# Performance work log

Hardware: AMD Instinct MI355X
Metric: run time of the kernel (lower is better)

Reference implementation:

```python
import jax, jax.numpy as jnp
import numpy as np

B, C, H, W, HEADS = 4, 32, 384, 384, 8
EPS_LN = 1e-6


def conv2d(x, w, b=None, pad=0, groups=1):
    out = jax.lax.conv_general_dilated(
        x, w, window_strides=(1, 1), padding=[(pad, pad), (pad, pad)],
        dimension_numbers=('NCHW', 'OIHW', 'NCHW'), feature_group_count=groups)
    return out if b is None else out + b[None, :, None, None]


def setup_inputs() -> dict:
    key = jax.random.key(0)
    ks = jax.random.split(key, 24)
    p = lambda k, shape: jax.random.normal(k, shape, jnp.float32) * 0.05
    return {
        'x': jax.random.normal(ks[0], (B, C, H, W), jnp.float32),
        # MCC core params (bias=False)
        'ln_w': jnp.ones((C,), jnp.float32),
        'ln_b': jnp.zeros((C,), jnp.float32),
        'temperature': jnp.ones((HEADS, 1, 1), jnp.float32),
        'pw_w': p(ks[1], (3 * C, C, 1, 1)),
        'dw_w': p(ks[2], (3 * C, 1, 3, 3)),
        'proj_w': p(ks[3], (C, C, 1, 1)),
        'ff1_w': p(ks[4], (C, C, 1, 1)),
        'ffdw_w': p(ks[5], (C, 1, 3, 3)),
        # color-space detector (convs have default bias=True)
        'det_w1': p(ks[6], (64, 32, 3, 3)), 'det_b1': jnp.zeros((64,), jnp.float32),
        'det_w2': p(ks[7], (128, 64, 3, 3)), 'det_b2': jnp.zeros((128,), jnp.float32),
        'det_w3': p(ks[8], (256, 128, 3, 3)), 'det_b3': jnp.zeros((256,), jnp.float32),
        'det_fc_w': p(ks[9], (3, 256)), 'det_fc_b': jnp.zeros((3,), jnp.float32),
        # HVI->RGB model
        'hvi_w1': p(ks[10], (64, 32, 3, 3)), 'hvi_b1': jnp.zeros((64,), jnp.float32),
        'hvi_w2': p(ks[11], (32, 64, 3, 3)), 'hvi_b2': jnp.zeros((32,), jnp.float32),
        # YCbCr->RGB model
        'ycc_w1': p(ks[12], (64, 32, 3, 3)), 'ycc_b1': jnp.zeros((64,), jnp.float32),
        'ycc_w2': p(ks[13], (32, 64, 3, 3)), 'ycc_b2': jnp.zeros((32,), jnp.float32),
    }


def _mcc_forward(x, ln_w, ln_b, temperature, pw_w, dw_w, proj_w, ff1_w, ffdw_w,
                 det_w1, det_b1, det_w2, det_b2, det_w3, det_b3, det_fc_w, det_fc_b,
                 hvi_w1, hvi_b1, hvi_w2, hvi_b2, ycc_w1, ycc_b1, ycc_w2, ycc_b2):
    relu = jax.nn.relu
    # ---- auto color-space detection ----
    f = relu(conv2d(x, det_w1, det_b1, pad=1))
    f = relu(conv2d(f, det_w2, det_b2, pad=1))
    f = relu(conv2d(f, det_w3, det_b3, pad=1))
    f = f.mean(axis=(2, 3))                      # adaptive avg pool -> [B, 256]
    logits = f @ det_fc_w.T + det_fc_b           # [B, 3]
    pred = jnp.argmax(logits[0])                 # torch uses predicted[0].item()

    def rgb_branch(xx):
        return xx

    def hvi_branch(xx):
        return relu(conv2d(relu(conv2d(xx, hvi_w1, hvi_b1, pad=1)), hvi_w2, hvi_b2, pad=1))

    def ycc_branch(xx):
        return relu(conv2d(relu(conv2d(xx, ycc_w1, ycc_b1, pad=1)), ycc_w2, ycc_b2, pad=1))

    x = jax.lax.switch(pred, [rgb_branch, hvi_branch, ycc_branch], x)

    # ---- channels_first LayerNorm ----
    u = x.mean(axis=1, keepdims=True)
    s = ((x - u) ** 2).mean(axis=1, keepdims=True)
    a = (x - u) / jnp.sqrt(s + EPS_LN)
    a = ln_w[None, :, None, None] * a + ln_b[None, :, None, None]

    # ---- qkv: 1x1 pwconv then 3x3 depthwise ----
    qkv = conv2d(conv2d(a, pw_w, pad=0), dw_w, pad=1, groups=3 * C)  # [B, 3C, H, W]
    q, k, v = jnp.split(qkv, 3, axis=1)
    ch = C // HEADS                                # channels per head
    hw = H * W
    q = q.reshape(B, HEADS, ch, hw)
    k = k.reshape(B, HEADS, ch, hw)
    v = v.reshape(B, HEADS, ch, hw)
    # L2-normalize over spatial dim (F.normalize, eps=1e-12)
    q = q / jnp.maximum(jnp.linalg.norm(q, axis=-1, keepdims=True), 1e-12)
    k = k / jnp.maximum(jnp.linalg.norm(k, axis=-1, keepdims=True), 1e-12)
    # channel-wise transposed attention: [B, heads, ch, ch]
    attn = jnp.einsum('bhcn,bhdn->bhcd', q, k) * temperature
    attn = jax.nn.softmax(attn, axis=-1)
    out = jnp.einsum('bhcd,bhdn->bhcn', attn, v).reshape(B, C, H, W)
    out = conv2d(out, proj_w, pad=0)

    # ---- feedforward on residual ----
    y = out + x
    y = jax.nn.gelu(conv2d(y, ff1_w, pad=0), approximate=False)
    y = jax.nn.gelu(conv2d(y, ffdw_w, pad=1, groups=C), approximate=False)
    return y


def reference(x, ln_w, ln_b, temperature, pw_w, dw_w, proj_w, ff1_w, ffdw_w,
              det_w1, det_b1, det_w2, det_b2, det_w3, det_b3, det_fc_w, det_fc_b,
              hvi_w1, hvi_b1, hvi_w2, hvi_b2, ycc_w1, ycc_b1, ycc_w2, ycc_b2):
    return _mcc_forward(x, ln_w, ln_b, temperature, pw_w, dw_w, proj_w, ff1_w, ffdw_w,
                        det_w1, det_b1, det_w2, det_b2, det_w3, det_b3, det_fc_w, det_fc_b,
                        hvi_w1, hvi_b1, hvi_w2, hvi_b2, ycc_w1, ycc_b1, ycc_w2, ycc_b2)
```

## Files before the change

### kernel.cpp

```cpp
#include <hip/hip_runtime.h>
#include <hip/hip_bf16.h>
#include <math.h>

#define HH 384
#define WW 384
#define HWSZ (HH*WW)
#define BB 4

typedef __attribute__((ext_vector_type(8))) short short8;
typedef __attribute__((ext_vector_type(4))) float f32x4;

static const size_t OFF_MISC = 0;
static const size_t OFF_A    = 16384;
static const size_t OFF_BW   = OFF_A + 56623104;
static const size_t MISC_POOLED = 0;
static const size_t MISC_PRED   = 1024;
static const size_t MISC_STATS  = 1056;
static const size_t MISC_MB     = 2048;

#define LPAD 40

__device__ __forceinline__ float waveSum(float v) {
#pragma unroll
    for (int off = 32; off > 0; off >>= 1) v += __shfl_down(v, off);
    return v;
}

__device__ __forceinline__ float gelu_exact(float v) {
    return 0.5f * v * (1.0f + erff(v * 0.70710678118654752f));
}

__device__ __forceinline__ unsigned short f2bf(float f) {
    __hip_bfloat16 h = __float2bfloat16(f);
    return *(unsigned short*)&h;
}
__device__ __forceinline__ float bf2f(unsigned short u) {
    unsigned int b = ((unsigned int)u) << 16;
    return __uint_as_float(b);
}

__device__ __forceinline__ void dwconv8(const float* __restrict__ base,
                                        const float* __restrict__ w9,
                                        int y, int xg, float o[8])
{
#pragma unroll
    for (int j = 0; j < 8; ++j) o[j] = 0.f;
#pragma unroll
    for (int dy = 0; dy < 3; ++dy) {
        int gy = y + dy - 1;
        if ((unsigned)gy >= (unsigned)HH) continue;
        const float* rp = base + (size_t)gy * WW + xg;
        f32x4 m0 = *(const f32x4*)(rp);
        f32x4 m1 = *(const f32x4*)(rp + 4);
        float r0 = (xg > 0) ? rp[-1] : 0.f;
        float r9 = (xg + 8 < WW) ? rp[8] : 0.f;
        float r[10] = {r0, m0[0], m0[1], m0[2], m0[3],
                           m1[0], m1[1], m1[2], m1[3], r9};
        float w0 = w9[dy * 3 + 0], w1 = w9[dy * 3 + 1], w2 = w9[dy * 3 + 2];
#pragma unroll
        for (int j = 0; j < 8; ++j)
            o[j] = fmaf(r[j], w0, fmaf(r[j + 1], w1, fmaf(r[j + 2], w2, o[j])));
    }
}


__global__ __launch_bounds__(256) void xcvt_kernel(
    const float* __restrict__ x, unsigned short* __restrict__ x0)
{
    int px = blockIdx.x * 256 + threadIdx.x;
    if (px >= HWSZ) return;
    unsigned short u[32];
#pragma unroll
    for (int c = 0; c < 32; ++c) u[c] = f2bf(x[(size_t)c * HWSZ + px]);
    uint4* dst = (uint4*)(x0 + (size_t)px * 32);
#pragma unroll
    for (int g = 0; g < 4; ++g) {
        uint4 v;
        v.x = (unsigned)u[g*8+0] | ((unsigned)u[g*8+1] << 16);
        v.y = (unsigned)u[g*8+2] | ((unsigned)u[g*8+3] << 16);
        v.z = (unsigned)u[g*8+4] | ((unsigned)u[g*8+5] << 16);
        v.w = (unsigned)u[g*8+6] | ((unsigned)u[g*8+7] << 16);
        dst[g] = v;
    }
}

__global__ __launch_bounds__(256) void wcvt_kernel(
    const float* __restrict__ w, unsigned short* __restrict__ wp,
    int Cin, int total)
{
    int t = blockIdx.x * 256 + threadIdx.x;
    if (t >= total) return;
    int nine_cin = 9 * Cin;
    int co = t / nine_cin;
    int r = t - co * nine_cin;
    int e = r / Cin;
    int ci = r - e * Cin;
    wp[t] = f2bf(w[(size_t)co * nine_cin + ci * 9 + e]);
}

template<int CIN, int COUT>
__global__ __launch_bounds__(256) void mfma_conv2_kernel(
    const unsigned short* __restrict__ in,
    const unsigned short* __restrict__ wp,
    const float* __restrict__ bias,
    unsigned short* __restrict__ out)
{
    constexpr int NT = COUT / 64;
    __shared__ unsigned short s_in[198 * LPAD];

    const int tid  = threadIdx.x;
    const int lane = tid & 63;
    const int wave = tid >> 6;
    const int nl   = lane & 15;
    const int quad = lane >> 4;
    const int row  = blockIdx.x / 6;
    const int x0   = (blockIdx.x % 6) * 64;
    const int co_w0 = wave * (COUT / 4);

    f32x4 acc[4][NT];
#pragma unroll
    for (int pg = 0; pg < 4; ++pg)
#pragma unroll
        for (int ct = 0; ct < NT; ++ct) acc[pg][ct] = (f32x4){0.f,0.f,0.f,0.f};

#pragma unroll
    for (int ci0 = 0; ci0 < CIN; ci0 += 32) {
        __syncthreads();
        for (int idx = tid; idx < 792; idx += 256) {
            int qs   = idx & 3;
            int cell = idx >> 2;
            int px   = cell % 66;
            int r    = cell / 66;
            int gy   = row + r - 1;
            int gx   = x0 + px - 1;
            uint4 v = {0u,0u,0u,0u};
            if ((unsigned)gy < (unsigned)HH && (unsigned)gx < (unsigned)WW)
                v = *(const uint4*)(in + (size_t)(gy * WW + gx) * CIN + ci0 + qs * 8);
            *(uint4*)(s_in + cell * LPAD + qs * 8) = v;
        }
        __syncthreads();
#pragma unroll
        for (int e = 0; e < 9; ++e) {
            const int er = e / 3, ec = e % 3;
            short8 bfrag[4];
#pragma unroll
            for (int pg = 0; pg < 4; ++pg)
                bfrag[pg] = *(const short8*)(s_in + ((er * 66 + pg * 16 + nl + ec) * LPAD + quad * 8));
#pragma unroll
            for (int ct = 0; ct < NT; ++ct) {
                short8 afrag = *(const short8*)(wp
                    + (size_t)(co_w0 + ct * 16 + nl) * (9 * CIN) + e * CIN + ci0 + quad * 8);
#pragma unroll
                for (int pg = 0; pg < 4; ++pg)
                    acc[pg][ct] = __builtin_amdgcn_mfma_f32_16x16x32_bf16(afrag, bfrag[pg], acc[pg][ct], 0, 0, 0);
            }
        }
    }

#pragma unroll
    for (int pg = 0; pg < 4; ++pg) {
        int px = x0 + pg * 16 + nl;
        unsigned short* op = out + ((size_t)row * WW + px) * COUT;
#pragma unroll
        for (int ct = 0; ct < NT; ++ct) {
            int cb = co_w0 + ct * 16 + quad * 4;
            ushort4 v;
            v.x = f2bf(fmaxf(acc[pg][ct][0] + bias[cb + 0], 0.f));
            v.y = f2bf(fmaxf(acc[pg][ct][1] + bias[cb + 1], 0.f));
            v.z = f2bf(fmaxf(acc[pg][ct][2] + bias[cb + 2], 0.f));
            v.w = f2bf(fmaxf(acc[pg][ct][3] + bias[cb + 3], 0.f));
            *(ushort4*)(op + cb) = v;
        }
    }
}

__global__ __launch_bounds__(256) void pool_kernel(
    const unsigned short* __restrict__ d3, float* __restrict__ pooled)
{
    __shared__ float s_pool[256];
    int t = threadIdx.x;
    s_pool[t] = 0.f;
    __syncthreads();
    int co8 = (t & 31) * 8;
    int pxg = t >> 5;
    float sums[8];
#pragma unroll
    for (int j = 0; j < 8; ++j) sums[j] = 0.f;
    int base = blockIdx.x * 2304 + pxg;
    for (int i = 0; i < 288; ++i) {
        int px = base + i * 8;
        const uint4* p = (const uint4*)(d3 + (size_t)px * 256 + co8);
        uint4 v = *p;
        unsigned int w[4] = {v.x, v.y, v.z, v.w};
#pragma unroll
        for (int g = 0; g < 4; ++g) {
            sums[g*2+0] += bf2f((unsigned short)(w[g] & 0xFFFF));
            sums[g*2+1] += bf2f((unsigned short)(w[g] >> 16));
        }
    }
#pragma unroll
    for (int j = 0; j < 8; ++j) atomicAdd(&s_pool[co8 + j], sums[j]);
    __syncthreads();
    atomicAdd(&pooled[t], s_pool[t]);
}

__global__ void fc_argmax_kernel(const float* __restrict__ pooled,
                                 const float* __restrict__ fcw,
                                 const float* __restrict__ fcb,
                                 int* __restrict__ pred)
{
    int t = threadIdx.x;
    float m = pooled[t] * (1.0f / (float)HWSZ);
    float p0 = m * fcw[t];
    float p1 = m * fcw[256 + t];
    float p2 = m * fcw[512 + t];
    p0 = waveSum(p0); p1 = waveSum(p1); p2 = waveSum(p2);
    __shared__ float rr[3][4];
    int wid = t >> 6, lane = t & 63;
    if (lane == 0) { rr[0][wid] = p0; rr[1][wid] = p1; rr[2][wid] = p2; }
    __syncthreads();
    if (t == 0) {
        float l0 = rr[0][0] + rr[0][1] + rr[0][2] + rr[0][3] + fcb[0];
        float l1 = rr[1][0] + rr[1][1] + rr[1][2] + rr[1][3] + fcb[1];
        float l2 = rr[2][0] + rr[2][1] + rr[2][2] + rr[2][3] + fcb[2];
        int best = 0; float bv = l0;
        if (l1 > bv) { best = 1; bv = l1; }
        if (l2 > bv) { best = 2; bv = l2; }
        *pred = best;
    }
}


__global__ __launch_bounds__(256) void wsplit_kernel(
    const float* __restrict__ w,
    unsigned short* __restrict__ hi, unsigned short* __restrict__ lo,
    int Cin, int total)
{
    int t = blockIdx.x * 256 + threadIdx.x;
    if (t >= total) return;
    int nine_cin = 9 * Cin;
    int co = t / nine_cin;
    int r = t - co * nine_cin;
    int e = r / Cin;
    int ci = r - e * Cin;
    float v = w[(size_t)co * nine_cin + ci * 9 + e];
    unsigned short h = f2bf(v);
    hi[t] = h;
    lo[t] = f2bf(v - bf2f(h));
}

__global__ __launch_bounds__(256) void xsplitb_kernel(
    const float* __restrict__ x, const int* __restrict__ predp,
    unsigned short* __restrict__ hi, unsigned short* __restrict__ lo)
{
    if (__builtin_amdgcn_readfirstlane(*predp) == 0) return;
    int p = blockIdx.x * 256 + threadIdx.x;
    if (p >= BB * HWSZ) return;
    int b = p / HWSZ, n = p % HWSZ;
    const float* sp = x + (size_t)b * 32 * HWSZ + n;
    unsigned short uh[32], ul[32];
#pragma unroll
    for (int c = 0; c < 32; ++c) {
        float v = sp[(size_t)c * HWSZ];
        unsigned short h = f2bf(v);
        uh[c] = h;
        ul[c] = f2bf(v - bf2f(h));
    }
    uint4* dh = (uint4*)(hi + (size_t)p * 32);
    uint4* dl = (uint4*)(lo + (size_t)p * 32);
#pragma unroll
    for (int g = 0; g < 4; ++g) {
        uint4 vh, vl;
        vh.x = (unsigned)uh[g*8+0] | ((unsigned)uh[g*8+1] << 16);
        vh.y = (unsigned)uh[g*8+2] | ((unsigned)uh[g*8+3] << 16);
        vh.z = (unsigned)uh[g*8+4] | ((unsigned)uh[g*8+5] << 16);
        vh.w = (unsigned)uh[g*8+6] | ((unsigned)uh[g*8+7] << 16);
        vl.x = (unsigned)ul[g*8+0] | ((unsigned)ul[g*8+1] << 16);
        vl.y = (unsigned)ul[g*8+2] | ((unsigned)ul[g*8+3] << 16);
        vl.z = (unsigned)ul[g*8+4] | ((unsigned)ul[g*8+5] << 16);
        vl.w = (unsigned)ul[g*8+6] | ((unsigned)ul[g*8+7] << 16);
        dh[g] = vh;
        dl[g] = vl;
    }
}

template<int CIN, int COUT, int OUTMODE>
__global__ __launch_bounds__(256) void bconv_kernel(
    const unsigned short* __restrict__ in_hi, const unsigned short* __restrict__ in_lo,
    const unsigned short* __restrict__ wAh, const unsigned short* __restrict__ wAl,
    const unsigned short* __restrict__ wBh, const unsigned short* __restrict__ wBl,
    const float* __restrict__ bA, const float* __restrict__ bB,
    const int* __restrict__ predp,
    unsigned short* __restrict__ out_hi, unsigned short* __restrict__ out_lo,
    float* __restrict__ out_f32)
{
    const int p = __builtin_amdgcn_readfirstlane(*predp);
    if (p == 0) return;
    const unsigned short* whi = (p == 1) ? wAh : wBh;
    const unsigned short* wlo = (p == 1) ? wAl : wBl;
    const float* bias = (p == 1) ? bA : bB;

    constexpr int NPG = (COUT == 64) ? 4 : 2;
    __shared__ unsigned short s_hi[198 * LPAD];
    __shared__ unsigned short s_lo[198 * LPAD];

    const int tid  = threadIdx.x;
    const int lane = tid & 63;
    const int wave = tid >> 6;
    const int nl   = lane & 15;
    const int quad = lane >> 4;
    const int row  = blockIdx.x / 6;
    const int x0   = (blockIdx.x % 6) * 64;
    const int b    = blockIdx.y;
    const int co_w0 = (COUT == 64) ? wave * 16 : (wave & 1) * 16;
    const int pg0   = (COUT == 64) ? 0 : (wave >> 1) * 2;

    f32x4 acc[NPG];
#pragma unroll
    for (int g = 0; g < NPG; ++g) acc[g] = (f32x4){0.f,0.f,0.f,0.f};

    const unsigned short* ibh = in_hi + (size_t)b * HWSZ * CIN;
    const unsigned short* ibl = in_lo + (size_t)b * HWSZ * CIN;

#pragma unroll
    for (int ci0 = 0; ci0 < CIN; ci0 += 32) {
        __syncthreads();
        for (int idx = tid; idx < 792; idx += 256) {
            int qs   = idx & 3;
            int cell = idx >> 2;
            int px   = cell % 66;
            int r    = cell / 66;
            int gy   = row + r - 1;
            int gx   = x0 + px - 1;
            uint4 vh = {0u,0u,0u,0u}, vl = {0u,0u,0u,0u};
            if ((unsigned)gy < (unsigned)HH && (unsigned)gx < (unsigned)WW) {
                size_t base = (size_t)(gy * WW + gx) * CIN + ci0 + qs * 8;
                vh = *(const uint4*)(ibh + base);
                vl = *(const uint4*)(ibl + base);
            }
            *(uint4*)(s_hi + cell * LPAD + qs * 8) = vh;
            *(uint4*)(s_lo + cell * LPAD + qs * 8) = vl;
        }
        __syncthreads();
#pragma unroll
        for (int e = 0; e < 9; ++e) {
            const int er = e / 3, ec = e % 3;
            size_t woff = (size_t)(co_w0 + nl) * (9 * CIN) + e * CIN + ci0 + quad * 8;
            short8 ah = *(const short8*)(whi + woff);
            short8 al = *(const short8*)(wlo + woff);
#pragma unroll
            for (int g = 0; g < NPG; ++g) {
                int cell = er * 66 + (pg0 + g) * 16 + nl + ec;
                short8 bh = *(const short8*)(s_hi + cell * LPAD + quad * 8);
                short8 bl = *(const short8*)(s_lo + cell * LPAD + quad * 8);
                acc[g] = __builtin_amdgcn_mfma_f32_16x16x32_bf16(ah, bh, acc[g], 0, 0, 0);
                acc[g] = __builtin_amdgcn_mfma_f32_16x16x32_bf16(ah, bl, acc[g], 0, 0, 0);
                acc[g] = __builtin_amdgcn_mfma_f32_16x16x32_bf16(al, bh, acc[g], 0, 0, 0);
            }
        }
    }

    const int cb = co_w0 + quad * 4;
#pragma unroll
    for (int g = 0; g < NPG; ++g) {
        int px = x0 + (pg0 + g) * 16 + nl;
        float r0 = fmaxf(acc[g][0] + bias[cb + 0], 0.f);
        float r1 = fmaxf(acc[g][1] + bias[cb + 1], 0.f);
        float r2 = fmaxf(acc[g][2] + bias[cb + 2], 0.f);
        float r3 = fmaxf(acc[g][3] + bias[cb + 3], 0.f);
        if (OUTMODE == 0) {
            size_t base = ((size_t)b * HWSZ + row * WW + px) * COUT + cb;
            ushort4 vh, vl;
            unsigned short h;
            h = f2bf(r0); vh.x = h; vl.x = f2bf(r0 - bf2f(h));
            h = f2bf(r1); vh.y = h; vl.y = f2bf(r1 - bf2f(h));
            h = f2bf(r2); vh.z = h; vl.z = f2bf(r2 - bf2f(h));
            h = f2bf(r3); vh.w = h; vl.w = f2bf(r3 - bf2f(h));
            *(ushort4*)(out_hi + base) = vh;
            *(ushort4*)(out_lo + base) = vl;
        } else {
            size_t sp = (size_t)row * WW + px;
            out_f32[((size_t)b * COUT + cb + 0) * HWSZ + sp] = r0;
            out_f32[((size_t)b * COUT + cb + 1) * HWSZ + sp] = r1;
            out_f32[((size_t)b * COUT + cb + 2) * HWSZ + sp] = r2;
            out_f32[((size_t)b * COUT + cb + 3) * HWSZ + sp] = r3;
        }
    }
}

__global__ __launch_bounds__(256) void lnpw_kernel(
    const float* __restrict__ x, const float* __restrict__ xb,
    const int* __restrict__ predp,
    const float* __restrict__ lnw, const float* __restrict__ lnb,
    const float* __restrict__ pww,
    float* __restrict__ qkvp)
{
    int p = blockIdx.x * 256 + threadIdx.x;
    if (p >= BB * HWSZ) return;
    int pr = __builtin_amdgcn_readfirstlane(*predp);
    const float* src = (pr == 0) ? x : xb;
    int b = p / HWSZ, n = p % HWSZ;
    const float* sp = src + (size_t)b * 32 * HWSZ + n;
    float v[32];
    float mean = 0.f;
#pragma unroll
    for (int c = 0; c < 32; ++c) { v[c] = sp[(size_t)c * HWSZ]; mean += v[c]; }
    mean *= (1.f / 32.f);
    float var = 0.f;
#pragma unroll
    for (int c = 0; c < 32; ++c) { float d = v[c] - mean; var += d * d; }
    var *= (1.f / 32.f);
    float rstd = rsqrtf(var + 1e-6f);
#pragma unroll
    for (int c = 0; c < 32; ++c)
        v[c] = (v[c] - mean) * rstd * lnw[c] + lnb[c];

    float acc[96];
#pragma unroll
    for (int co = 0; co < 96; ++co) acc[co] = 0.f;
    for (int ci = 0; ci < 32; ++ci) {
        float va = v[ci];
#pragma unroll
        for (int co = 0; co < 96; ++co)
            acc[co] = fmaf(pww[co * 32 + ci], va, acc[co]);
    }
    float* op = qkvp + (size_t)b * 96 * HWSZ + n;
#pragma unroll
    for (int co = 0; co < 96; ++co) op[(size_t)co * HWSZ] = acc[co];
}

__global__ __launch_bounds__(256) void qkdwstats_kernel(
    const float* __restrict__ qkvp, const float* __restrict__ dww,
    float* __restrict__ stats)
{
    int bh = blockIdx.y;
    int b = bh >> 3, h = bh & 7;
    const float* qbase = qkvp + ((size_t)b * 96 + h * 4) * HWSZ;
    const float* kbase = qkvp + ((size_t)b * 96 + 32 + h * 4) * HWSZ;
    const float* wq = dww + (h * 4) * 9;
    const float* wk = dww + (32 + h * 4) * 9;

    int g = blockIdx.x * 256 + threadIdx.x;
    int y  = g / 48;
    int xg = (g - y * 48) * 8;

    float s[16], qn[4], kn[4];
#pragma unroll
    for (int i = 0; i < 16; ++i) s[i] = 0.f;
#pragma unroll
    for (int i = 0; i < 4; ++i) { qn[i] = 0.f; kn[i] = 0.f; }

    float q[4][8];
#pragma unroll
    for (int c = 0; c < 4; ++c) {
        dwconv8(qbase + (size_t)c * HWSZ, wq + c * 9, y, xg, q[c]);
#pragma unroll
        for (int j = 0; j < 8; ++j) qn[c] = fmaf(q[c][j], q[c][j], qn[c]);
    }
#pragma unroll
    for (int d = 0; d < 4; ++d) {
        float k[8];
        dwconv8(kbase + (size_t)d * HWSZ, wk + d * 9, y, xg, k);
#pragma unroll
        for (int j = 0; j < 8; ++j) kn[d] = fmaf(k[j], k[j], kn[d]);
#pragma unroll
        for (int c = 0; c < 4; ++c)
#pragma unroll
            for (int j = 0; j < 8; ++j)
                s[c * 4 + d] = fmaf(q[c][j], k[j], s[c * 4 + d]);
    }

    float* st = stats + bh * 24;
    int lane = threadIdx.x & 63;
#pragma unroll
    for (int i = 0; i < 16; ++i) {
        float v = waveSum(s[i]);
        if (lane == 0) atomicAdd(&st[i], v);
    }
#pragma unroll
    for (int i = 0; i < 4; ++i) {
        float v = waveSum(qn[i]);
        if (lane == 0) atomicAdd(&st[16 + i], v);
        float u = waveSum(kn[i]);
        if (lane == 0) atomicAdd(&st[20 + i], u);
    }
}

__global__ __launch_bounds__(256) void vdw_kernel(
    float* __restrict__ qkvp, const float* __restrict__ dww)
{
    int t = blockIdx.x * 256 + threadIdx.x;
    int bc = t / 18432;
    int g  = t - bc * 18432;
    int b = bc >> 5, c = bc & 31;
    int y  = g / 48;
    int xg = (g - y * 48) * 8;
    const float* ip = qkvp + ((size_t)b * 96 + 64 + c) * HWSZ;
    const float* wc = dww + (64 + c) * 9;
    float o[8];
    dwconv8(ip, wc, y, xg, o);
    float* op = qkvp + ((size_t)b * 96 + c) * HWSZ + (size_t)y * WW + xg;
    f32x4 v0 = {o[0], o[1], o[2], o[3]};
    f32x4 v1 = {o[4], o[5], o[6], o[7]};
    *(f32x4*)op = v0;
    *(f32x4*)(op + 4) = v1;
}

__global__ void attnmb_kernel(const float* __restrict__ stats,
                              const float* __restrict__ temp,
                              const float* __restrict__ projw,
                              float* __restrict__ Mb)
{
    __shared__ float attn_s[4][8][4][4];
    int t = threadIdx.x;
    if (t < 128) {
        int b = t >> 5;
        int h = (t >> 2) & 7;
        int c = t & 3;
        const float* st = stats + (b * 8 + h) * 24;
        float qn = fmaxf(sqrtf(st[16 + c]), 1e-12f);
        float tp = temp[h];
        float raw[4];
#pragma unroll
        for (int d = 0; d < 4; ++d) {
            float kn = fmaxf(sqrtf(st[20 + d]), 1e-12f);
            raw[d] = st[c * 4 + d] / (qn * kn) * tp;
        }
        float m = fmaxf(fmaxf(raw[0], raw[1]), fmaxf(raw[2], raw[3]));
        float e0 = expf(raw[0] - m), e1 = expf(raw[1] - m);
        float e2 = expf(raw[2] - m), e3 = expf(raw[3] - m);
        float inv = 1.f / (e0 + e1 + e2 + e3);
        attn_s[b][h][c][0] = e0 * inv;
        attn_s[b][h][c][1] = e1 * inv;
        attn_s[b][h][c][2] = e2 * inv;
        attn_s[b][h][c][3] = e3 * inv;
    }
    __syncthreads();
    for (int idx = t; idx < 4096; idx += 256) {
        int b = idx >> 10;
        int r = idx & 1023;
        int co = r >> 5;
        int j = r & 31;
        int h = j >> 2;
        int d = j & 3;
        float m = 0.f;
#pragma unroll
        for (int l = 0; l < 4; ++l)
            m = fmaf(projw[co * 32 + h * 4 + l], attn_s[b][h][l][d], m);
        Mb[idx] = m;
    }
}

__global__ __launch_bounds__(256) void e1_kernel(
    float* __restrict__ qkvp, const float* __restrict__ x,
    const float* __restrict__ xb, const int* __restrict__ predp,
    const float* __restrict__ Mb, const float* __restrict__ ff1w)
{
    int p = blockIdx.x * 256 + threadIdx.x;
    if (p >= BB * HWSZ) return;
    int pr = __builtin_amdgcn_readfirstlane(*predp);
    const float* src = (pr == 0) ? x : xb;
    int b = p / HWSZ, n = p % HWSZ;
    float* vp = qkvp + (size_t)b * 96 * HWSZ + n;
    const float* Mbb = Mb + b * 1024;
    float y[32];
#pragma unroll
    for (int c = 0; c < 32; ++c) y[c] = 0.f;
    for (int j = 0; j < 32; ++j) {
        float vj = vp[(size_t)j * HWSZ];
#pragma unroll
        for (int co = 0; co < 32; ++co)
            y[co] = fmaf(Mbb[co * 32 + j], vj, y[co]);
    }
    const float* xp = src + (size_t)b * 32 * HWSZ + n;
#pragma unroll
    for (int c = 0; c < 32; ++c) y[c] += xp[(size_t)c * HWSZ];
    for (int co = 0; co < 32; ++co) {
        float s = 0.f;
#pragma unroll
        for (int ci = 0; ci < 32; ++ci)
            s = fmaf(ff1w[co * 32 + ci], y[ci], s);
        vp[(size_t)co * HWSZ] = gelu_exact(s);
    }
}

__global__ __launch_bounds__(256) void fdw_kernel(
    const float* __restrict__ z1, const float* __restrict__ w,
    float* __restrict__ out)
{
    int t = blockIdx.x * 256 + threadIdx.x;
    int bc = t / 18432;
    int g  = t - bc * 18432;
    int b = bc >> 5, c = bc & 31;
    int y  = g / 48;
    int xg = (g - y * 48) * 8;
    const float* ip = z1 + ((size_t)b * 96 + c) * HWSZ;
    const float* wc = w + c * 9;
    float o[8];
    dwconv8(ip, wc, y, xg, o);
#pragma unroll
    for (int j = 0; j < 8; ++j) o[j] = gelu_exact(o[j]);
    float* op = out + ((size_t)b * 32 + c) * HWSZ + (size_t)y * WW + xg;
    f32x4 v0 = {o[0], o[1], o[2], o[3]};
    f32x4 v1 = {o[4], o[5], o[6], o[7]};
    *(f32x4*)op = v0;
    *(f32x4*)(op + 4) = v1;
}

extern "C" void kernel_launch(void* const* d_in, const int* in_sizes, int n_in,
                              void* d_out, int out_size, void* d_ws, size_t ws_size,
                              hipStream_t stream)
{
    (void)in_sizes; (void)n_in; (void)out_size; (void)ws_size;
    const float* x      = (const float*)d_in[0];
    const float* ln_w   = (const float*)d_in[1];
    const float* ln_b   = (const float*)d_in[2];
    const float* temp   = (const float*)d_in[3];
    const float* pw_w   = (const float*)d_in[4];
    const float* dw_w   = (const float*)d_in[5];
    const float* proj_w = (const float*)d_in[6];
    const float* ff1_w  = (const float*)d_in[7];
    const float* ffdw_w = (const float*)d_in[8];
    const float* det_w1 = (const float*)d_in[9];
    const float* det_b1 = (const float*)d_in[10];
    const float* det_w2 = (const float*)d_in[11];
    const float* det_b2 = (const float*)d_in[12];
    const float* det_w3 = (const float*)d_in[13];
    const float* det_b3 = (const float*)d_in[14];
    const float* fc_w   = (const float*)d_in[15];
    const float* fc_b   = (const float*)d_in[16];
    const float* hvi_w1 = (const float*)d_in[17];
    const float* hvi_b1 = (const float*)d_in[18];
    const float* hvi_w2 = (const float*)d_in[19];
    const float* hvi_b2 = (const float*)d_in[20];
    const float* ycc_w1 = (const float*)d_in[21];
    const float* ycc_b1 = (const float*)d_in[22];
    const float* ycc_w2 = (const float*)d_in[23];
    const float* ycc_b2 = (const float*)d_in[24];

    float* ws     = (float*)d_ws;
    float* misc   = ws + OFF_MISC;
    float* A      = ws + OFF_A;
    unsigned short* x0bf  = (unsigned short*)A;
    unsigned short* f1bf  = (unsigned short*)(A + 2359296);
    unsigned short* f2bf  = (unsigned short*)(A + 7077888);
    unsigned short* d3out = (unsigned short*)(A + 16515072);
    unsigned short* w1p   = (unsigned short*)(A + 56423104);
    unsigned short* w2p   = (unsigned short*)(A + 56432320);
    unsigned short* w3p   = (unsigned short*)(A + 56469184);
    unsigned short* xs_hi = (unsigned short*)A;
    unsigned short* xs_lo = (unsigned short*)(A + 9437184);
    unsigned short* t1_hi = (unsigned short*)(A + 18874368);
    unsigned short* t1_lo = (unsigned short*)(A + 37748736);
    unsigned short* bw    = (unsigned short*)(ws + OFF_BW);
    unsigned short* bw_h1h = bw;            unsigned short* bw_h1l = bw + 18432;
    unsigned short* bw_y1h = bw + 36864;    unsigned short* bw_y1l = bw + 55296;
    unsigned short* bw_h2h = bw + 73728;    unsigned short* bw_h2l = bw + 92160;
    unsigned short* bw_y2h = bw + 110592;   unsigned short* bw_y2l = bw + 129024;
    float* qkvp   = A;
    float* xb     = (float*)d_out;
    float* pooled = misc + MISC_POOLED;
    int*   pred   = (int*)(misc + MISC_PRED);
    float* stats  = misc + MISC_STATS;
    float* Mb     = misc + MISC_MB;
    float* out    = (float*)d_out;

    hipMemsetAsync(misc, 0, 2048 * sizeof(float), stream);

    dim3 blk(256);
    wcvt_kernel<<<(18432 + 255) / 256, blk, 0, stream>>>(det_w1, w1p, 32, 18432);
    wcvt_kernel<<<(73728 + 255) / 256, blk, 0, stream>>>(det_w2, w2p, 64, 73728);
    wcvt_kernel<<<(294912 + 255) / 256, blk, 0, stream>>>(det_w3, w3p, 128, 294912);
    xcvt_kernel<<<576, blk, 0, stream>>>(x, x0bf);
    wsplit_kernel<<<72, blk, 0, stream>>>(hvi_w1, bw_h1h, bw_h1l, 32, 18432);
    wsplit_kernel<<<72, blk, 0, stream>>>(ycc_w1, bw_y1h, bw_y1l, 32, 18432);
    wsplit_kernel<<<72, blk, 0, stream>>>(hvi_w2, bw_h2h, bw_h2l, 64, 18432);
    wsplit_kernel<<<72, blk, 0, stream>>>(ycc_w2, bw_y2h, bw_y2l, 64, 18432);

    mfma_conv2_kernel<32, 64>  <<<2304, blk, 0, stream>>>(x0bf, w1p, det_b1, f1bf);
    mfma_conv2_kernel<64, 128> <<<2304, blk, 0, stream>>>(f1bf, w2p, det_b2, f2bf);
    mfma_conv2_kernel<128, 256><<<2304, blk, 0, stream>>>(f2bf, w3p, det_b3, d3out);
    pool_kernel<<<64, blk, 0, stream>>>(d3out, pooled);
    fc_argmax_kernel<<<1, 256, 0, stream>>>(pooled, fc_w, fc_b, pred);

    xsplitb_kernel<<<2304, blk, 0, stream>>>(x, pred, xs_hi, xs_lo);
    bconv_kernel<32, 64, 0><<<dim3(2304, BB), blk, 0, stream>>>(
        xs_hi, xs_lo, bw_h1h, bw_h1l, bw_y1h, bw_y1l, hvi_b1, ycc_b1, pred,
        t1_hi, t1_lo, nullptr);
    bconv_kernel<64, 32, 1><<<dim3(2304, BB), blk, 0, stream>>>(
        t1_hi, t1_lo, bw_h2h, bw_h2l, bw_y2h, bw_y2l, hvi_b2, ycc_b2, pred,
        nullptr, nullptr, xb);

    lnpw_kernel<<<2304, blk, 0, stream>>>(x, xb, pred, ln_w, ln_b, pw_w, qkvp);

    qkdwstats_kernel<<<dim3(72, 32), blk, 0, stream>>>(qkvp, dw_w, stats);
    vdw_kernel<<<9216, blk, 0, stream>>>(qkvp, dw_w);
    attnmb_kernel<<<1, 256, 0, stream>>>(stats, temp, proj_w, Mb);

    e1_kernel<<<2304, blk, 0, stream>>>(qkvp, x, xb, pred, Mb, ff1_w);
    fdw_kernel<<<9216, blk, 0, stream>>>(qkvp, ffdw_w, out);
}
```

Before: 1.316 ms.

## Halve per-thread width in qk depthwise stats kernel and double-buffer row loads

Each thread in the q/k depthwise-conv + Gram statistics kernel now handles 4 pixels instead of 8, so the grid doubles to 144x32 blocks. Loads use clamped branchless row reads and are software-pipelined with two register buffers, so the next channel's rows are fetched while the current one is convolved. A launch-bounds occupancy hint of 4 is added. The aim is more parallelism and latency hiding in this memory-bound kernel. The cost is more halo reloads per pixel and twice as many wave reductions and atomics.

```diff
diff --git a/kernel.cpp b/kernel.cpp
--- a/kernel.cpp
+++ b/kernel.cpp
@@ -59,6 +59,42 @@
         float w0 = w9[dy * 3 + 0], w1 = w9[dy * 3 + 1], w2 = w9[dy * 3 + 2];
 #pragma unroll
         for (int j = 0; j < 8; ++j)
+            o[j] = fmaf(r[j], w0, fmaf(r[j + 1], w1, fmaf(r[j + 2], w2, o[j])));
+    }
+}
+
+__device__ __forceinline__ void dwload4v(const float* __restrict__ base,
+                                         int y, int xg,
+                                         f32x4 m[3], float e0[3], float e1[3])
+{
+#pragma unroll
+    for (int dy = 0; dy < 3; ++dy) {
+        int gy = y + dy - 1;
+        int cy = gy < 0 ? 0 : (gy > HH - 1 ? HH - 1 : gy);
+        const float* rp = base + (size_t)cy * WW + xg;
+        f32x4 v = *(const f32x4*)rp;
+        float a = rp[xg > 0 ? -1 : 0];
+        float bvl = rp[xg + 4 < WW ? 4 : 3];
+        bool ok = (unsigned)gy < (unsigned)HH;
+        m[dy]  = ok ? v : (f32x4){0.f, 0.f, 0.f, 0.f};
+        e0[dy] = (ok && xg > 0)      ? a   : 0.f;
+        e1[dy] = (ok && xg + 4 < WW) ? bvl : 0.f;
+    }
+}
+
+__device__ __forceinline__ void dwapply4v(const f32x4 m[3], const float e0[3],
+                                          const float e1[3],
+                                          const float* __restrict__ w9,
+                                          float o[4])
+{
+#pragma unroll
+    for (int j = 0; j < 4; ++j) o[j] = 0.f;
+#pragma unroll
+    for (int dy = 0; dy < 3; ++dy) {
+        float r[6] = {e0[dy], m[dy][0], m[dy][1], m[dy][2], m[dy][3], e1[dy]};
+        float w0 = w9[dy * 3 + 0], w1 = w9[dy * 3 + 1], w2 = w9[dy * 3 + 2];
+#pragma unroll
+        for (int j = 0; j < 4; ++j)
             o[j] = fmaf(r[j], w0, fmaf(r[j + 1], w1, fmaf(r[j + 2], w2, o[j])));
     }
 }
@@ -429,7 +465,7 @@
     for (int co = 0; co < 96; ++co) op[(size_t)co * HWSZ] = acc[co];
 }
 
-__global__ __launch_bounds__(256) void qkdwstats_kernel(
+__global__ __launch_bounds__(256, 4) void qkdwstats_kernel(
     const float* __restrict__ qkvp, const float* __restrict__ dww,
     float* __restrict__ stats)
 {
@@ -441,8 +477,8 @@
     const float* wk = dww + (32 + h * 4) * 9;
 
     int g = blockIdx.x * 256 + threadIdx.x;
-    int y  = g / 48;
-    int xg = (g - y * 48) * 8;
+    int y  = g / 96;
+    int xg = (g - y * 96) * 4;
 
     float s[16], qn[4], kn[4];
 #pragma unroll
@@ -450,25 +486,59 @@
 #pragma unroll
     for (int i = 0; i < 4; ++i) { qn[i] = 0.f; kn[i] = 0.f; }
 
-    float q[4][8];
-#pragma unroll
-    for (int c = 0; c < 4; ++c) {
-        dwconv8(qbase + (size_t)c * HWSZ, wq + c * 9, y, xg, q[c]);
-#pragma unroll
-        for (int j = 0; j < 8; ++j) qn[c] = fmaf(q[c][j], q[c][j], qn[c]);
-    }
-#pragma unroll
-    for (int d = 0; d < 4; ++d) {
-        float k[8];
-        dwconv8(kbase + (size_t)d * HWSZ, wk + d * 9, y, xg, k);
-#pragma unroll
-        for (int j = 0; j < 8; ++j) kn[d] = fmaf(k[j], k[j], kn[d]);
-#pragma unroll
-        for (int c = 0; c < 4; ++c)
-#pragma unroll
-            for (int j = 0; j < 8; ++j)
-                s[c * 4 + d] = fmaf(q[c][j], k[j], s[c * 4 + d]);
-    }
+    f32x4 mA[3]; float eA0[3], eA1[3];
+    f32x4 mB[3]; float eB0[3], eB1[3];
+    float q[4][4];
+    float k4[4];
+
+    dwload4v(qbase,                  y, xg, mA, eA0, eA1);
+    dwload4v(qbase + (size_t)HWSZ,   y, xg, mB, eB0, eB1);
+    dwapply4v(mA, eA0, eA1, wq + 0,  q[0]);
+    dwload4v(qbase + (size_t)2*HWSZ, y, xg, mA, eA0, eA1);
+    dwapply4v(mB, eB0, eB1, wq + 9,  q[1]);
+    dwload4v(qbase + (size_t)3*HWSZ, y, xg, mB, eB0, eB1);
+    dwapply4v(mA, eA0, eA1, wq + 18, q[2]);
+    dwload4v(kbase,                  y, xg, mA, eA0, eA1);
+    dwapply4v(mB, eB0, eB1, wq + 27, q[3]);
+#pragma unroll
+    for (int c = 0; c < 4; ++c)
+#pragma unroll
+        for (int j = 0; j < 4; ++j) qn[c] = fmaf(q[c][j], q[c][j], qn[c]);
+
+    dwload4v(kbase + (size_t)HWSZ,   y, xg, mB, eB0, eB1);
+    dwapply4v(mA, eA0, eA1, wk + 0, k4);
+#pragma unroll
+    for (int j = 0; j < 4; ++j) kn[0] = fmaf(k4[j], k4[j], kn[0]);
+#pragma unroll
+    for (int c = 0; c < 4; ++c)
+#pragma unroll
+        for (int j = 0; j < 4; ++j) s[c*4+0] = fmaf(q[c][j], k4[j], s[c*4+0]);
+
+    dwload4v(kbase + (size_t)2*HWSZ, y, xg, mA, eA0, eA1);
+    dwapply4v(mB, eB0, eB1, wk + 9, k4);
+#pragma unroll
+    for (int j = 0; j < 4; ++j) kn[1] = fmaf(k4[j], k4[j], kn[1]);
+#pragma unroll
+    for (int c = 0; c < 4; ++c)
+#pragma unroll
+        for (int j = 0; j < 4; ++j) s[c*4+1] = fmaf(q[c][j], k4[j], s[c*4+1]);
+
+    dwload4v(kbase + (size_t)3*HWSZ, y, xg, mB, eB0, eB1);
+    dwapply4v(mA, eA0, eA1, wk + 18, k4);
+#pragma unroll
+    for (int j = 0; j < 4; ++j) kn[2] = fmaf(k4[j], k4[j], kn[2]);
+#pragma unroll
+    for (int c = 0; c < 4; ++c)
+#pragma unroll
+        for (int j = 0; j < 4; ++j) s[c*4+2] = fmaf(q[c][j], k4[j], s[c*4+2]);
+
+    dwapply4v(mB, eB0, eB1, wk + 27, k4);
+#pragma unroll
+    for (int j = 0; j < 4; ++j) kn[3] = fmaf(k4[j], k4[j], kn[3]);
+#pragma unroll
+    for (int c = 0; c < 4; ++c)
+#pragma unroll
+        for (int j = 0; j < 4; ++j) s[c*4+3] = fmaf(q[c][j], k4[j], s[c*4+3]);
 
     float* st = stats + bh * 24;
     int lane = threadIdx.x & 63;
@@ -693,7 +763,7 @@
 
     lnpw_kernel<<<2304, blk, 0, stream>>>(x, xb, pred, ln_w, ln_b, pw_w, qkvp);
 
-    qkdwstats_kernel<<<dim3(72, 32), blk, 0, stream>>>(qkvp, dw_w, stats);
+    qkdwstats_kernel<<<dim3(144, 32), blk, 0, stream>>>(qkvp, dw_w, stats);
     vdw_kernel<<<9216, blk, 0, stream>>>(qkvp, dw_w);
     attnmb_kernel<<<1, 256, 0, stream>>>(stats, temp, proj_w, Mb);
 
```

Result: slower. 1.661 ms (+26.2%).
